# Performance work log

Hardware: AMD Instinct MI355X
Metric: run time of the kernel (lower is better)

The kernel has to match this reference:

```python
import jax, jax.numpy as jnp
import numpy as np
import math

D_MODEL = 2048
N_HEADS = 16
HEAD_DIM = 128
ROPE_THETA = 10000.0


def apply_rope(x, pos, theta=ROPE_THETA):
    # x: [b, h, s, d], pos: [b, s] int
    d = x.shape[-1]
    inv_freq = 1.0 / (theta ** (jnp.arange(0, d, 2, dtype=jnp.float32) / d))  # [d/2]
    ang = pos.astype(jnp.float32)[:, None, :, None] * inv_freq  # [b,1,s,d/2]
    cos, sin = jnp.cos(ang), jnp.sin(ang)
    x1, x2 = x[..., 0::2], x[..., 1::2]
    out_even = x1 * cos - x2 * sin
    out_odd = x1 * sin + x2 * cos
    return jnp.stack([out_even, out_odd], axis=-1).reshape(x.shape)


def setup_inputs() -> dict:
    key = jax.random.key(0)
    ks = jax.random.split(key, 5)
    b, s = 2, 2048
    scale = 1.0 / math.sqrt(D_MODEL)
    x = jax.random.normal(ks[0], (b, s, D_MODEL), dtype=jnp.float32)
    Wq = jax.random.normal(ks[1], (D_MODEL, D_MODEL), dtype=jnp.float32) * scale
    Wk = jax.random.normal(ks[2], (D_MODEL, D_MODEL), dtype=jnp.float32) * scale
    Wv = jax.random.normal(ks[3], (D_MODEL, D_MODEL), dtype=jnp.float32) * scale
    Wo = jax.random.normal(ks[4], (D_MODEL, D_MODEL), dtype=jnp.float32) * scale
    token_positions = jnp.broadcast_to(jnp.arange(s, dtype=jnp.int32), (b, s))
    return {"x": x, "token_positions": token_positions, "Wq": Wq, "Wk": Wk, "Wv": Wv, "Wo": Wo}


def reference(x, token_positions, Wq, Wk, Wv, Wo):
    b, s, _ = x.shape
    h, d = N_HEADS, HEAD_DIM
    # QKV projections (Linear: x @ W.T), split heads: b s (h d) -> b h s d
    def proj(W):
        y = jnp.einsum('bse,fe->bsf', x, W)
        return y.reshape(b, s, h, d).transpose(0, 2, 1, 3)
    Q, K, V = proj(Wq), proj(Wk), proj(Wv)
    Q = apply_rope(Q, token_positions)
    K = apply_rope(K, token_positions)
    logits = jnp.einsum('bhqd,bhkd->bhqk', Q, K) / math.sqrt(d)
    causal = jnp.triu(jnp.ones((s, s), dtype=bool), 1)
    logits = jnp.where(causal, -jnp.inf, logits)
    attn = jax.nn.softmax(logits, axis=-1)
    ctx = jnp.einsum('bhqk,bhkd->bhqd', attn, V)
    ctx = ctx.transpose(0, 2, 1, 3).reshape(b, s, h * d)
    return jnp.einsum('bsf,ef->bse', ctx, Wo)
```

## Files before the change

### kernel.cpp

```cpp
#include <hip/hip_runtime.h>
#include <cstdint>
#include <cstddef>

typedef __bf16 bf16_t;
typedef __bf16 bf16x8 __attribute__((ext_vector_type(8)));
typedef float  f32x4  __attribute__((ext_vector_type(4)));

#define SEQ 2048
#define NH  16
#define HD  128
#define MM  4096
#define KK  2048

#define ASYNC16(g, l) __builtin_amdgcn_global_load_lds( \
    (const __attribute__((address_space(1))) void*)(g), \
    (__attribute__((address_space(3))) void*)(l), 16, 0, 0)

__global__ __launch_bounds__(256) void cast_all(const float* __restrict__ x,
                                                const float* __restrict__ Wq,
                                                const float* __restrict__ Wk,
                                                const float* __restrict__ Wv,
                                                const float* __restrict__ Wo,
                                                bf16_t* __restrict__ xb,
                                                bf16_t* __restrict__ wqkv,
                                                bf16_t* __restrict__ wob) {
    int i = blockIdx.x * 256 + threadIdx.x;
    const float* src;
    bf16_t* dst;
    int off;
    if (i < 2097152) { src = x; dst = xb; off = i; }
    else {
        int j = i - 2097152;
        int sel = j >> 20; off = j & 0xFFFFF;
        if (sel < 3) { src = (sel == 0) ? Wq : (sel == 1) ? Wk : Wv; dst = wqkv + (size_t)sel * 4194304; }
        else         { src = Wo; dst = wob; }
    }
    float4 v = ((const float4*)src)[off];
    union { bf16_t h[4]; uint2 u; } t;
    t.h[0] = (bf16_t)v.x; t.h[1] = (bf16_t)v.y;
    t.h[2] = (bf16_t)v.z; t.h[3] = (bf16_t)v.w;
    ((uint2*)dst)[off] = t.u;
}

template<int MODE>
__global__ __launch_bounds__(256) void gemm_bt(const bf16_t* __restrict__ A,
                                               const bf16_t* __restrict__ B,
                                               void* __restrict__ Cout,
                                               bf16_t* __restrict__ Kout,
                                               bf16_t* __restrict__ Vout,
                                               const int* __restrict__ pos) {
    __shared__ union SMem {
        struct { bf16_t A[8 * 512]; bf16_t B[8 * 512]; } st;
        bf16_t epi[64 * 136];
    } sm;

    const int tid = threadIdx.x;
    const int w = tid >> 6, l = tid & 63;
    const int lane16 = l & 15, quad = l >> 4;
    const int tm = blockIdx.y, tn = blockIdx.x;
    const int wm = w >> 1, wn = w & 1;

    const bf16_t* pA0 = A + (size_t)(tm * 128 + (2 * w + 0) * 16 + lane16) * KK + quad * 8;
    const bf16_t* pA1 = A + (size_t)(tm * 128 + (2 * w + 1) * 16 + lane16) * KK + quad * 8;
    const bf16_t* pB0 = B + (size_t)(tn * 128 + (2 * w + 0) * 16 + lane16) * KK + quad * 8;
    const bf16_t* pB1 = B + (size_t)(tn * 128 + (2 * w + 1) * 16 + lane16) * KK + quad * 8;

    bf16_t* wA0 = &sm.st.A[(2 * w + 0) * 512];
    bf16_t* wA1 = &sm.st.A[(2 * w + 1) * 512];
    bf16_t* wB0 = &sm.st.B[(2 * w + 0) * 512];
    bf16_t* wB1 = &sm.st.B[(2 * w + 1) * 512];
    const bf16_t* rA = &sm.st.A[wm * 4 * 512 + l * 8];
    const bf16_t* rB = &sm.st.B[wn * 4 * 512 + l * 8];

    f32x4 acc[4][4];
    for (int i = 0; i < 4; i++)
        for (int j = 0; j < 4; j++) acc[i][j] = (f32x4){0.f, 0.f, 0.f, 0.f};

    for (int k0 = 0; k0 < KK; k0 += 32) {
        __syncthreads();
        ASYNC16(pA0, wA0); ASYNC16(pA1, wA1);
        ASYNC16(pB0, wB0); ASYNC16(pB1, wB1);
        pA0 += 32; pA1 += 32; pB0 += 32; pB1 += 32;
        __syncthreads();
        bf16x8 af[4], bfr[4];
        for (int i = 0; i < 4; i++) af[i]  = *(const bf16x8*)(rA + i * 512);
        for (int j = 0; j < 4; j++) bfr[j] = *(const bf16x8*)(rB + j * 512);
        for (int i = 0; i < 4; i++)
            for (int j = 0; j < 4; j++)
                acc[i][j] = __builtin_amdgcn_mfma_f32_16x16x32_bf16(af[i], bfr[j], acc[i][j], 0, 0, 0);
    }

    if (MODE == 1) {
        const int mbase = tm * 128 + wm * 64;
        const int nbase = tn * 128 + wn * 64;
        for (int i = 0; i < 4; i++)
            for (int j = 0; j < 4; j++) {
                const int n  = nbase + j * 16 + lane16;
                const int m0 = mbase + i * 16 + quad * 4;
                for (int r = 0; r < 4; r++)
                    ((float*)Cout)[(size_t)(m0 + r) * 2048 + n] = acc[i][j][r];
            }
        return;
    }

    const int mbase = tm * 128;
    const int nb    = tn * 128;
    const int sel   = nb >> 11;
    const int hh    = (nb & 2047) >> 7;
    const int bidx  = mbase >> 11;
    const int g  = tid >> 4;
    const int c8 = (tid & 15) * 8;

    if (sel < 2) {
        bf16_t* dstbase = ((sel == 0) ? (bf16_t*)Cout : Kout) +
                          (size_t)(bidx * NH + hh) * SEQ * HD;
        const float qs = (sel == 0) ? 0.08838834764831845f : 1.0f;
        for (int half = 0; half < 2; half++) {
            __syncthreads();
            if (wm == half) {
                for (int i = 0; i < 4; i++)
                    for (int j = 0; j < 4; j++)
                        for (int r = 0; r < 4; r++)
                            sm.epi[(i * 16 + quad * 4 + r) * 136 + wn * 64 + j * 16 + lane16] =
                                (bf16_t)acc[i][j][r];
            }
            __syncthreads();
            for (int p = 0; p < 4; p++) {
                const int rid = p * 16 + g;
                const int s = (mbase & 2047) + half * 64 + rid;
                bf16x8 v = *(const bf16x8*)&sm.epi[rid * 136 + c8];
                const float pp = (float)pos[bidx * SEQ + s];
                union { bf16_t h8[8]; uint4 u; } o;
                for (int t = 0; t < 4; t++) {
                    const int fi = (c8 >> 1) + t;
                    const float freq = exp2f(-(float)fi * 0.20762050593045857f);
                    const float ang = pp * freq;
                    const float sn = __sinf(ang), cs = __cosf(ang);
                    const float x1 = (float)v[2 * t], x2 = (float)v[2 * t + 1];
                    o.h8[2 * t]     = (bf16_t)((x1 * cs - x2 * sn) * qs);
                    o.h8[2 * t + 1] = (bf16_t)((x1 * sn + x2 * cs) * qs);
                }
                *(uint4*)(dstbase + (size_t)s * HD + c8) = o.u;
            }
        }
    } else {
        bf16_t* dstb = Vout + (size_t)(bidx * NH + hh) * HD * SEQ;
        const int s0 = mbase & 2047;
        for (int half = 0; half < 2; half++) {
            __syncthreads();
            if (wn == half) {
                for (int i = 0; i < 4; i++)
                    for (int j = 0; j < 4; j++) {
                        union { bf16_t h4[4]; uint2 u; } pk;
                        for (int r = 0; r < 4; r++) pk.h4[r] = (bf16_t)acc[i][j][r];
                        *(uint2*)&sm.epi[(j * 16 + lane16) * 136 + wm * 64 + i * 16 + quad * 4] = pk.u;
                    }
            }
            __syncthreads();
            for (int p = 0; p < 4; p++) {
                const int rid = p * 16 + g;
                const int d = half * 64 + rid;
                bf16x8 v = *(const bf16x8*)&sm.epi[rid * 136 + c8];
                *(uint4*)(dstb + (size_t)d * SEQ + s0 + c8) = *(const uint4*)&v;
            }
        }
    }
}

__global__ __launch_bounds__(256) void attn_kernel(const bf16_t* __restrict__ Q,
                                                   const bf16_t* __restrict__ K,
                                                   const bf16_t* __restrict__ Vt,
                                                   bf16_t* __restrict__ ctx) {
    const int flat = blockIdx.x;
    const int bh = flat & 31;
    const int bt = flat >> 5;
    const int h = bh & 15, b = bh >> 4;
    const bf16_t* Qh = Q  + (size_t)bh * SEQ * HD;
    const bf16_t* Kh = K  + (size_t)bh * SEQ * HD;
    const bf16_t* Vh = Vt + (size_t)bh * HD * SEQ;

    const int tid = threadIdx.x;
    const int w = tid >> 6, l = tid & 63;
    const int lane16 = l & 15, quad = l >> 4;

    __shared__ bf16_t kt[2][16 * 512];
    __shared__ bf16_t vt[2][16 * 512];
    __shared__ bf16_t pbuf[4][1024];

    for (int half = 0; half < 2; half++) {
        const int qt = half ? (31 - bt) : bt;
        const int q0 = qt * 64 + w * 16;

        bf16x8 qf[4];
        {
            const bf16_t* qrow = Qh + (size_t)(q0 + lane16) * HD + quad * 8;
            for (int kc = 0; kc < 4; kc++) qf[kc] = *(const bf16x8*)(qrow + kc * 32);
        }

        f32x4 o[8];
        for (int dt = 0; dt < 8; dt++) o[dt] = (f32x4){0.f, 0.f, 0.f, 0.f};
        float m_s = -INFINITY, l_s = 0.f;

        __syncthreads();
        for (int ii = 0; ii < 4; ii++) {
            const int f = w * 4 + ii;
            const int nt = f >> 2, kc = f & 3;
            ASYNC16(Kh + (size_t)(nt * 16 + lane16) * HD + kc * 32 + quad * 8, &kt[0][f * 512]);
            const int dt = f >> 1, kk = f & 1;
            ASYNC16(Vh + (size_t)(dt * 16 + lane16) * SEQ + kk * 32 + quad * 8, &vt[0][f * 512]);
        }

        int cur = 0;
        for (int kb = 0; kb <= qt; kb++) {
            const int k0 = kb * 64;
            __syncthreads();
            if (kb < qt) {
                const int kn = k0 + 64;
                for (int ii = 0; ii < 4; ii++) {
                    const int f = w * 4 + ii;
                    const int nt = f >> 2, kc = f & 3;
                    ASYNC16(Kh + (size_t)(kn + nt * 16 + lane16) * HD + kc * 32 + quad * 8,
                            &kt[1 - cur][f * 512]);
                    const int dt = f >> 1, kk = f & 1;
                    ASYNC16(Vh + (size_t)(dt * 16 + lane16) * SEQ + kn + kk * 32 + quad * 8,
                            &vt[1 - cur][f * 512]);
                }
            }
            const bf16_t* ktc = kt[cur];
            const bf16_t* vtc = vt[cur];

            f32x4 sacc[4];
            for (int nt = 0; nt < 4; nt++) sacc[nt] = (f32x4){0.f, 0.f, 0.f, 0.f};
            for (int nt = 0; nt < 4; nt++)
                for (int kc = 0; kc < 4; kc++) {
                    bf16x8 kf = *(const bf16x8*)&ktc[(nt * 4 + kc) * 512 + l * 8];
                    sacc[nt] = __builtin_amdgcn_mfma_f32_16x16x32_bf16(kf, qf[kc], sacc[nt], 0, 0, 0);
                }
            if (kb == qt) {
                const int qg = q0 + lane16;
                for (int nt = 0; nt < 4; nt++)
                    for (int r = 0; r < 4; r++) {
                        const int kg = k0 + nt * 16 + quad * 4 + r;
                        if (kg > qg) sacc[nt][r] = -INFINITY;
                    }
            }
            float rowmax = sacc[0][0];
            for (int nt = 0; nt < 4; nt++)
                for (int r = 0; r < 4; r++) rowmax = fmaxf(rowmax, sacc[nt][r]);
            rowmax = fmaxf(rowmax, __shfl_xor(rowmax, 16, 64));
            rowmax = fmaxf(rowmax, __shfl_xor(rowmax, 32, 64));
            const float mnew = fmaxf(m_s, rowmax);
            const float a = __expf(m_s - mnew);
            m_s = mnew;
            float ssum = 0.f;
            for (int nt = 0; nt < 4; nt++) {
                union { bf16_t h4[4]; uint2 u; } pk;
                for (int r = 0; r < 4; r++) {
                    const float e = __expf(sacc[nt][r] - mnew);
                    ssum += e;
                    pk.h4[r] = (bf16_t)e;
                }
                const int addr = (nt >> 1) * 512 +
                                 (((nt & 1) * 2 + (quad >> 1)) * 16 + lane16) * 8 +
                                 (quad & 1) * 4;
                *(uint2*)&pbuf[w][addr] = pk.u;
            }
            ssum += __shfl_xor(ssum, 16, 64);
            ssum += __shfl_xor(ssum, 32, 64);
            l_s = l_s * a + ssum;

            float ar[4];
            for (int r = 0; r < 4; r++) ar[r] = __shfl(a, (quad << 2) | r, 16);
            for (int dt = 0; dt < 8; dt++)
                for (int r = 0; r < 4; r++) o[dt][r] *= ar[r];
            for (int kk = 0; kk < 2; kk++) {
                bf16x8 pf = *(const bf16x8*)&pbuf[w][kk * 512 + l * 8];
                for (int dt = 0; dt < 8; dt++) {
                    bf16x8 vf = *(const bf16x8*)&vtc[(dt * 2 + kk) * 512 + l * 8];
                    o[dt] = __builtin_amdgcn_mfma_f32_16x16x32_bf16(pf, vf, o[dt], 0, 0, 0);
                }
            }
            cur ^= 1;
        }

        float inv[4];
        for (int r = 0; r < 4; r++) inv[r] = 1.0f / __shfl(l_s, (quad << 2) | r, 16);
        for (int r = 0; r < 4; r++) {
            const int qg = q0 + quad * 4 + r;
            bf16_t* dst = ctx + ((size_t)(b * SEQ + qg)) * (NH * HD) + h * HD;
            for (int dt = 0; dt < 8; dt++)
                dst[dt * 16 + lane16] = (bf16_t)(o[dt][r] * inv[r]);
        }
        __syncthreads();
    }
}

extern "C" void kernel_launch(void* const* d_in, const int* in_sizes, int n_in,
                              void* d_out, int out_size, void* d_ws, size_t ws_size,
                              hipStream_t stream) {
    const float* x  = (const float*)d_in[0];
    const int* pos  = (const int*)d_in[1];
    const float* Wq = (const float*)d_in[2];
    const float* Wk = (const float*)d_in[3];
    const float* Wv = (const float*)d_in[4];
    const float* Wo = (const float*)d_in[5];

    char* ws = (char*)d_ws;
    bf16_t* xb   = (bf16_t*)(ws);
    bf16_t* wqkv = (bf16_t*)(ws + (16u << 20));
    bf16_t* wob  = (bf16_t*)(ws + (40u << 20));
    bf16_t* Qb   = (bf16_t*)(ws + (48u << 20));
    bf16_t* Kb   = (bf16_t*)(ws + (64u << 20));
    bf16_t* Vt   = (bf16_t*)(ws + (80u << 20));
    bf16_t* ctx  = (bf16_t*)(ws + (96u << 20));

    cast_all<<<24576, 256, 0, stream>>>(x, Wq, Wk, Wv, Wo, xb, wqkv, wob);

    dim3 gq(6144 / 128, MM / 128);
    gemm_bt<3><<<gq, 256, 0, stream>>>(xb, wqkv, (void*)Qb, Kb, Vt, pos);

    attn_kernel<<<512, 256, 0, stream>>>(Qb, Kb, Vt, ctx);

    dim3 gg(2048 / 128, MM / 128);
    gemm_bt<1><<<gg, 256, 0, stream>>>(ctx, wob, d_out, nullptr, nullptr, nullptr);
}
```

Before: 471.1 us.

## Replace LDS-staged GEMM with single-wave 64x64 tiles loading directly to registers

Both projection GEMMs now launch one 64-thread wave per 64x64 output tile. Operand fragments are read straight from global memory into registers and prefetched one k-step ahead, replacing the LDS staging and its two barriers per iteration. This removes the synchronisation cost but drops data reuse across waves, so global and L2 traffic per FLOP roughly doubles. It also quadruples the block count, and the QKV epilogue uses a smaller single-wave shared buffer.

```diff
diff --git a/kernel.cpp b/kernel.cpp
--- a/kernel.cpp
+++ b/kernel.cpp
@@ -42,57 +42,51 @@
     ((uint2*)dst)[off] = t.u;
 }
 
+#define MFMA16(a, b, c) __builtin_amdgcn_mfma_f32_16x16x32_bf16(a, b, c, 0, 0, 0)
+
 template<int MODE>
-__global__ __launch_bounds__(256) void gemm_bt(const bf16_t* __restrict__ A,
-                                               const bf16_t* __restrict__ B,
-                                               void* __restrict__ Cout,
-                                               bf16_t* __restrict__ Kout,
-                                               bf16_t* __restrict__ Vout,
-                                               const int* __restrict__ pos) {
-    __shared__ union SMem {
-        struct { bf16_t A[8 * 512]; bf16_t B[8 * 512]; } st;
-        bf16_t epi[64 * 136];
-    } sm;
-
-    const int tid = threadIdx.x;
-    const int w = tid >> 6, l = tid & 63;
+__device__ __forceinline__ void gemm_body(bf16_t* __restrict__ epi,
+                                          const bf16_t* __restrict__ A,
+                                          const bf16_t* __restrict__ B,
+                                          void* __restrict__ Cout,
+                                          bf16_t* __restrict__ Kout,
+                                          bf16_t* __restrict__ Vout,
+                                          const int* __restrict__ pos) {
+    const int l = threadIdx.x;
     const int lane16 = l & 15, quad = l >> 4;
     const int tm = blockIdx.y, tn = blockIdx.x;
-    const int wm = w >> 1, wn = w & 1;
-
-    const bf16_t* pA0 = A + (size_t)(tm * 128 + (2 * w + 0) * 16 + lane16) * KK + quad * 8;
-    const bf16_t* pA1 = A + (size_t)(tm * 128 + (2 * w + 1) * 16 + lane16) * KK + quad * 8;
-    const bf16_t* pB0 = B + (size_t)(tn * 128 + (2 * w + 0) * 16 + lane16) * KK + quad * 8;
-    const bf16_t* pB1 = B + (size_t)(tn * 128 + (2 * w + 1) * 16 + lane16) * KK + quad * 8;
-
-    bf16_t* wA0 = &sm.st.A[(2 * w + 0) * 512];
-    bf16_t* wA1 = &sm.st.A[(2 * w + 1) * 512];
-    bf16_t* wB0 = &sm.st.B[(2 * w + 0) * 512];
-    bf16_t* wB1 = &sm.st.B[(2 * w + 1) * 512];
-    const bf16_t* rA = &sm.st.A[wm * 4 * 512 + l * 8];
-    const bf16_t* rB = &sm.st.B[wn * 4 * 512 + l * 8];
+
+    const bf16_t* pa[4];
+    const bf16_t* pb[4];
+    for (int i = 0; i < 4; i++) {
+        pa[i] = A + (size_t)(tm * 64 + i * 16 + lane16) * KK + quad * 8;
+        pb[i] = B + (size_t)(tn * 64 + i * 16 + lane16) * KK + quad * 8;
+    }
 
     f32x4 acc[4][4];
     for (int i = 0; i < 4; i++)
         for (int j = 0; j < 4; j++) acc[i][j] = (f32x4){0.f, 0.f, 0.f, 0.f};
 
-    for (int k0 = 0; k0 < KK; k0 += 32) {
-        __syncthreads();
-        ASYNC16(pA0, wA0); ASYNC16(pA1, wA1);
-        ASYNC16(pB0, wB0); ASYNC16(pB1, wB1);
-        pA0 += 32; pA1 += 32; pB0 += 32; pB1 += 32;
-        __syncthreads();
-        bf16x8 af[4], bfr[4];
-        for (int i = 0; i < 4; i++) af[i]  = *(const bf16x8*)(rA + i * 512);
-        for (int j = 0; j < 4; j++) bfr[j] = *(const bf16x8*)(rB + j * 512);
+    bf16x8 a[4], b[4];
+    for (int i = 0; i < 4; i++) a[i] = *(const bf16x8*)pa[i];
+    for (int i = 0; i < 4; i++) b[i] = *(const bf16x8*)pb[i];
+
+    for (int k0 = 32; k0 < KK; k0 += 32) {
+        bf16x8 an[4], bn[4];
+        for (int i = 0; i < 4; i++) an[i] = *(const bf16x8*)(pa[i] + k0);
+        for (int i = 0; i < 4; i++) bn[i] = *(const bf16x8*)(pb[i] + k0);
         for (int i = 0; i < 4; i++)
             for (int j = 0; j < 4; j++)
-                acc[i][j] = __builtin_amdgcn_mfma_f32_16x16x32_bf16(af[i], bfr[j], acc[i][j], 0, 0, 0);
-    }
+                acc[i][j] = MFMA16(a[i], b[j], acc[i][j]);
+        for (int i = 0; i < 4; i++) { a[i] = an[i]; b[i] = bn[i]; }
+    }
+    for (int i = 0; i < 4; i++)
+        for (int j = 0; j < 4; j++)
+            acc[i][j] = MFMA16(a[i], b[j], acc[i][j]);
 
     if (MODE == 1) {
-        const int mbase = tm * 128 + wm * 64;
-        const int nbase = tn * 128 + wn * 64;
+        const int mbase = tm * 64;
+        const int nbase = tn * 64;
         for (int i = 0; i < 4; i++)
             for (int j = 0; j < 4; j++) {
                 const int n  = nbase + j * 16 + lane16;
@@ -103,68 +97,69 @@
         return;
     }
 
-    const int mbase = tm * 128;
-    const int nb    = tn * 128;
-    const int sel   = nb >> 11;
-    const int hh    = (nb & 2047) >> 7;
-    const int bidx  = mbase >> 11;
-    const int g  = tid >> 4;
-    const int c8 = (tid & 15) * 8;
+    const int n0   = tn * 64;
+    const int sel  = n0 >> 11;
+    const int hh   = (n0 & 2047) >> 7;
+    const int d0   = n0 & 127;
+    const int m0g  = tm * 64;
+    const int bidx = m0g >> 11;
+    const int s0   = m0g & 2047;
+    const int rl = l >> 3, c = (l & 7) * 8;
 
     if (sel < 2) {
-        bf16_t* dstbase = ((sel == 0) ? (bf16_t*)Cout : Kout) +
-                          (size_t)(bidx * NH + hh) * SEQ * HD;
+        for (int i = 0; i < 4; i++)
+            for (int j = 0; j < 4; j++)
+                for (int r = 0; r < 4; r++)
+                    epi[(i * 16 + quad * 4 + r) * 68 + j * 16 + lane16] = (bf16_t)acc[i][j][r];
         const float qs = (sel == 0) ? 0.08838834764831845f : 1.0f;
-        for (int half = 0; half < 2; half++) {
-            __syncthreads();
-            if (wm == half) {
-                for (int i = 0; i < 4; i++)
-                    for (int j = 0; j < 4; j++)
-                        for (int r = 0; r < 4; r++)
-                            sm.epi[(i * 16 + quad * 4 + r) * 136 + wn * 64 + j * 16 + lane16] =
-                                (bf16_t)acc[i][j][r];
-            }
-            __syncthreads();
-            for (int p = 0; p < 4; p++) {
-                const int rid = p * 16 + g;
-                const int s = (mbase & 2047) + half * 64 + rid;
-                bf16x8 v = *(const bf16x8*)&sm.epi[rid * 136 + c8];
-                const float pp = (float)pos[bidx * SEQ + s];
-                union { bf16_t h8[8]; uint4 u; } o;
-                for (int t = 0; t < 4; t++) {
-                    const int fi = (c8 >> 1) + t;
-                    const float freq = exp2f(-(float)fi * 0.20762050593045857f);
-                    const float ang = pp * freq;
-                    const float sn = __sinf(ang), cs = __cosf(ang);
-                    const float x1 = (float)v[2 * t], x2 = (float)v[2 * t + 1];
-                    o.h8[2 * t]     = (bf16_t)((x1 * cs - x2 * sn) * qs);
-                    o.h8[2 * t + 1] = (bf16_t)((x1 * sn + x2 * cs) * qs);
-                }
-                *(uint4*)(dstbase + (size_t)s * HD + c8) = o.u;
-            }
+        bf16_t* dst = ((sel == 0) ? (bf16_t*)Cout : Kout) + (size_t)(bidx * NH + hh) * SEQ * HD;
+        for (int p = 0; p < 8; p++) {
+            const int row = p * 8 + rl;
+            const int s = s0 + row;
+            bf16x8 v = *(const bf16x8*)&epi[row * 68 + c];
+            const float pp = (float)pos[bidx * SEQ + s];
+            union { bf16_t h8[8]; uint4 u; } o;
+            for (int t = 0; t < 4; t++) {
+                const int fi = ((d0 + c) >> 1) + t;
+                const float freq = exp2f(-(float)fi * 0.20762050593045857f);
+                const float ang = pp * freq;
+                const float sn = __sinf(ang), cs = __cosf(ang);
+                const float x1 = (float)v[2 * t], x2 = (float)v[2 * t + 1];
+                o.h8[2 * t]     = (bf16_t)((x1 * cs - x2 * sn) * qs);
+                o.h8[2 * t + 1] = (bf16_t)((x1 * sn + x2 * cs) * qs);
+            }
+            *(uint4*)(dst + (size_t)s * HD + d0 + c) = o.u;
         }
     } else {
-        bf16_t* dstb = Vout + (size_t)(bidx * NH + hh) * HD * SEQ;
-        const int s0 = mbase & 2047;
-        for (int half = 0; half < 2; half++) {
-            __syncthreads();
-            if (wn == half) {
-                for (int i = 0; i < 4; i++)
-                    for (int j = 0; j < 4; j++) {
-                        union { bf16_t h4[4]; uint2 u; } pk;
-                        for (int r = 0; r < 4; r++) pk.h4[r] = (bf16_t)acc[i][j][r];
-                        *(uint2*)&sm.epi[(j * 16 + lane16) * 136 + wm * 64 + i * 16 + quad * 4] = pk.u;
-                    }
-            }
-            __syncthreads();
-            for (int p = 0; p < 4; p++) {
-                const int rid = p * 16 + g;
-                const int d = half * 64 + rid;
-                bf16x8 v = *(const bf16x8*)&sm.epi[rid * 136 + c8];
-                *(uint4*)(dstb + (size_t)d * SEQ + s0 + c8) = *(const uint4*)&v;
-            }
-        }
-    }
+        for (int i = 0; i < 4; i++)
+            for (int j = 0; j < 4; j++) {
+                union { bf16_t h4[4]; uint2 u; } pk;
+                for (int r = 0; r < 4; r++) pk.h4[r] = (bf16_t)acc[i][j][r];
+                *(uint2*)&epi[(j * 16 + lane16) * 68 + i * 16 + quad * 4] = pk.u;
+            }
+        bf16_t* dst = Vout + (size_t)(bidx * NH + hh) * HD * SEQ;
+        for (int p = 0; p < 8; p++) {
+            const int drow = p * 8 + rl;
+            bf16x8 v = *(const bf16x8*)&epi[drow * 68 + c];
+            *(uint4*)(dst + (size_t)(d0 + drow) * SEQ + s0 + c) = *(const uint4*)&v;
+        }
+    }
+}
+
+__global__ __launch_bounds__(64, 3) void gemm_qkv(const bf16_t* __restrict__ A,
+                                                  const bf16_t* __restrict__ B,
+                                                  bf16_t* __restrict__ Qout,
+                                                  bf16_t* __restrict__ Kout,
+                                                  bf16_t* __restrict__ Vout,
+                                                  const int* __restrict__ pos) {
+    __shared__ bf16_t epi[64 * 68];
+    gemm_body<3>(epi, A, B, (void*)Qout, Kout, Vout, pos);
+}
+
+__global__ __launch_bounds__(64, 3) void gemm_out(const bf16_t* __restrict__ A,
+                                                  const bf16_t* __restrict__ B,
+                                                  float* __restrict__ Cout) {
+    gemm_body<1>(nullptr, A, B, (void*)Cout, nullptr, nullptr, nullptr);
 }
 
 __global__ __launch_bounds__(256) void attn_kernel(const bf16_t* __restrict__ Q,
@@ -316,11 +311,11 @@
 
     cast_all<<<24576, 256, 0, stream>>>(x, Wq, Wk, Wv, Wo, xb, wqkv, wob);
 
-    dim3 gq(6144 / 128, MM / 128);
-    gemm_bt<3><<<gq, 256, 0, stream>>>(xb, wqkv, (void*)Qb, Kb, Vt, pos);
+    dim3 gq(6144 / 64, MM / 64);
+    gemm_qkv<<<gq, 64, 0, stream>>>(xb, wqkv, Qb, Kb, Vt, pos);
 
     attn_kernel<<<512, 256, 0, stream>>>(Qb, Kb, Vt, ctx);
 
-    dim3 gg(2048 / 128, MM / 128);
-    gemm_bt<1><<<gg, 256, 0, stream>>>(ctx, wob, d_out, nullptr, nullptr, nullptr);
-}
+    dim3 gg(2048 / 64, MM / 64);
+    gemm_out<<<gg, 64, 0, stream>>>(ctx, wob, (float*)d_out);
+}
```

New measurement: 677.0 us. +43.7%, slower.
